# Performance work log

Hardware: AMD Instinct MI355X
Metric: run time of the kernel (lower is better)

The kernel has to match this reference:

```python
import jax, jax.numpy as jnp
import numpy as np

B, T, D, H, NHASH, BS, L, DFF = 4, 4096, 512, 8, 4, 64, 4, 2048
DH = D // H           # 64
NB = T // BS          # 64 buckets per hash round
MASK_VAL = -5e4       # TOKEN_SELF_ATTN_VALUE from reformer-pytorch


def setup_inputs() -> dict:
    key = jax.random.key(0)
    ks = jax.random.split(key, 8)
    s = D ** -0.5
    return {
        "src": jax.random.normal(ks[0], (B, T, D), jnp.float32),
        "rotations": jax.random.normal(ks[1], (L, DH, NHASH, NB // 2), jnp.float32),
        "Wqk": jax.random.normal(ks[2], (L, D, D), jnp.float32) * s,
        "Wv": jax.random.normal(ks[3], (L, D, D), jnp.float32) * s,
        "Wout": jax.random.normal(ks[4], (L, D, D), jnp.float32) * s,
        "bout": jnp.zeros((L, D), jnp.float32),
        "W1": jax.random.normal(ks[5], (L, DFF, D), jnp.float32) * s,
        "b1": jnp.zeros((L, DFF), jnp.float32),
        "W2": jax.random.normal(ks[6], (L, D, DFF), jnp.float32) * (DFF ** -0.5),
        "b2": jnp.zeros((L, D), jnp.float32),
        "g2": jnp.ones((L, D), jnp.float32),
        "be2": jnp.zeros((L, D), jnp.float32),
        "gf": jnp.ones((D,), jnp.float32),
        "bf": jnp.zeros((D,), jnp.float32),
    }


def _ln(x, g, b, eps=1e-6):
    m = x.mean(-1, keepdims=True)
    v = ((x - m) ** 2).mean(-1, keepdims=True)
    return (x - m) * jax.lax.rsqrt(v + eps) * g + b


def _look_one_back(x):
    # concat each chunk with the previous chunk along the within-chunk axis
    return jnp.concatenate([x, jnp.roll(x, 1, axis=1)], axis=2)


def _lsh_attention(qk, v, rot):
    # qk, v: (bh, T, DH); rot: (DH, NHASH, NB//2). Shared-QK LSH attention.
    bh = qk.shape[0]
    rotated = jnp.einsum('btf,fhr->bhtr', qk, rot)               # (bh,NHASH,T,NB/2)
    full = jnp.concatenate([rotated, -rotated], axis=-1)          # (bh,NHASH,T,NB)
    buckets = jnp.argmax(full, axis=-1)                           # (bh,NHASH,T)
    buckets = buckets + (jnp.arange(NHASH) * NB)[None, :, None]   # offset per round
    buckets = buckets.reshape(bh, NHASH * T)

    ticker = jnp.arange(NHASH * T)
    bt = buckets * T + (ticker % T)                               # unique sort keys
    sticker = jnp.argsort(bt, axis=-1)                            # sort positions
    undo = jnp.argsort(sticker, axis=-1)
    st = sticker % T                                              # original positions

    sqk = jnp.take_along_axis(qk, st[..., None], axis=1)          # (bh,NHASH*T,DH)
    sv = jnp.take_along_axis(v, st[..., None], axis=1)

    C = NHASH * NB                                                # chunks
    bq_t = st.reshape(bh, C, BS)
    bqk = sqk.reshape(bh, C, BS, DH)
    bv = sv.reshape(bh, C, BS, DH)

    bq = bqk
    bk = bqk / jnp.maximum(jnp.linalg.norm(bqk, axis=-1, keepdims=True), 1e-12)
    bk = _look_one_back(bk)                                       # (bh,C,2*BS,DH)
    bv = _look_one_back(bv)
    bkv_t = _look_one_back(bq_t)                                  # (bh,C,2*BS)

    dots = jnp.einsum('bcie,bcje->bcij', bq, bk) * (DH ** -0.5)   # (bh,C,BS,2BS)
    self_mask = bq_t[:, :, :, None] == bkv_t[:, :, None, :]
    dots = jnp.where(self_mask, MASK_VAL, dots)

    lse = jax.scipy.special.logsumexp(dots, axis=-1, keepdims=True)
    probs = jnp.exp(dots - lse)
    bo = jnp.einsum('bcij,bcje->bcie', probs, bv)                 # (bh,C,BS,DH)

    so = bo.reshape(bh, NHASH * T, DH)
    slog = lse.reshape(bh, NHASH * T)
    o = jnp.take_along_axis(so, undo[..., None], axis=1).reshape(bh, NHASH, T, DH)
    lg = jnp.take_along_axis(slog, undo, axis=1).reshape(bh, NHASH, T, 1)
    w = jnp.exp(lg - jax.scipy.special.logsumexp(lg, axis=1, keepdims=True))
    return jnp.sum(o * w, axis=1)                                 # (bh,T,DH)


def _split_heads(x):
    return x.reshape(B, T, H, DH).transpose(0, 2, 1, 3).reshape(B * H, T, DH)


def _merge_heads(x):
    return x.reshape(B, H, T, DH).transpose(0, 2, 1, 3).reshape(B, T, D)


def reference(src, rotations, Wqk, Wv, Wout, bout, W1, b1, W2, b2, g2, be2, gf, bf):
    x = src
    for i in range(L):
        # LSH self-attention (post-norm path: norm1 is never applied in source)
        qk = _split_heads(x @ Wqk[i].T)
        v = _split_heads(x @ Wv[i].T)
        att = _merge_heads(_lsh_attention(qk, v, rotations[i]))
        att = att @ Wout[i].T + bout[i]
        x = x + att
        # positionalwise FFN + residual + norm2
        ff = jax.nn.relu(x @ W1[i].T + b1[i]) @ W2[i].T + b2[i]
        x = _ln(x + ff, g2[i], be2[i])
    return _ln(x, gf, bf)
```

## Files before the change

### kernel.cpp

```cpp
#include <hip/hip_runtime.h>
#include <math.h>

#define TT    4096
#define DD    512
#define HH    8
#define DHH   64
#define NH    4
#define LLAY  4
#define DFFN  2048
#define BHH   32
#define NC    256
#define MROWS 16384

typedef __attribute__((ext_vector_type(8))) short s16x8;
typedef __attribute__((ext_vector_type(4))) float f32x4;
typedef unsigned short ushort_t;

union U4 { unsigned u[4]; s16x8 v; };

__device__ __forceinline__ unsigned short f2bf(float f) {
    unsigned u = __float_as_uint(f);
    unsigned r = (u + 0x7FFFu + ((u >> 16) & 1u)) >> 16;
    return (unsigned short)r;
}
__device__ __forceinline__ float bf2f(unsigned short h) {
    return __uint_as_float(((unsigned)h) << 16);
}

__device__ __forceinline__ void xcd_swz(int& bx, int& by) {
    const int gx = gridDim.x;
    const int nwg = gx * gridDim.y;
    const int flat = by * gx + bx;
    const int q = nwg >> 3;
    const int swz = (flat & 7) * q + (flat >> 3);
    bx = swz % gx;
    by = swz / gx;
}

__global__ __launch_bounds__(256) void gemm_bf3_k(
    const ushort_t* __restrict__ Ah, const ushort_t* __restrict__ Al, int lda,
    const ushort_t* __restrict__ Wh, const ushort_t* __restrict__ Wl, int ldw,
    const float* __restrict__ bias, const float* __restrict__ resid,
    float* __restrict__ outf, ushort_t* __restrict__ outh, ushort_t* __restrict__ outl,
    unsigned* __restrict__ outp,
    int M, int N, int K, int relu)
{
    __shared__ __align__(16) ushort_t lds[2][4 * 128 * 32];
    const int tid  = threadIdx.x;
    const int lane = tid & 63;
    const int wv   = tid >> 6;
    const int wm   = wv >> 1, wn = wv & 1;
    int bx = blockIdx.x, by = blockIdx.y;
    xcd_swz(bx, by);
    const int row0 = by * 128, col0 = bx * 128;
    const int g    = lane >> 4;
    const int srow0 = wv * 32;

    f32x4 acc[4][4];
#pragma unroll
    for (int mi = 0; mi < 4; mi++)
#pragma unroll
        for (int ni = 0; ni < 4; ni++) acc[mi][ni] = (f32x4)(0.f);

    auto STAGE = [&](int buf, int k0) {
#pragma unroll
        for (int ii = 0; ii < 2; ii++) {
            const int r   = srow0 + ii * 16 + (lane >> 2);
            const int ug  = (((lane & 3) ^ ((r >> 1) & 3)) << 3);
            const size_t ga = (size_t)(row0 + r) * lda + k0 + ug;
            const size_t gw = (size_t)(col0 + r) * ldw + k0 + ug;
            const int lo  = (srow0 + ii * 16) * 32;
            __builtin_amdgcn_global_load_lds(
                (const __attribute__((address_space(1))) void*)(Ah + ga),
                (__attribute__((address_space(3))) void*)&lds[buf][0 * 4096 + lo], 16, 0, 0);
            __builtin_amdgcn_global_load_lds(
                (const __attribute__((address_space(1))) void*)(Al + ga),
                (__attribute__((address_space(3))) void*)&lds[buf][1 * 4096 + lo], 16, 0, 0);
            __builtin_amdgcn_global_load_lds(
                (const __attribute__((address_space(1))) void*)(Wh + gw),
                (__attribute__((address_space(3))) void*)&lds[buf][2 * 4096 + lo], 16, 0, 0);
            __builtin_amdgcn_global_load_lds(
                (const __attribute__((address_space(1))) void*)(Wl + gw),
                (__attribute__((address_space(3))) void*)&lds[buf][3 * 4096 + lo], 16, 0, 0);
        }
    };

    const int nt = K >> 5;
    STAGE(0, 0);

    for (int t = 0; t < nt; ++t) {
        const int cur = t & 1;
        if (t + 1 < nt) {
            STAGE(cur ^ 1, (t + 1) << 5);
            asm volatile("s_waitcnt vmcnt(8)" ::: "memory");
        } else {
            asm volatile("s_waitcnt vmcnt(0)" ::: "memory");
        }
        __builtin_amdgcn_s_barrier();
        __builtin_amdgcn_sched_barrier(0);

        s16x8 ah[4], al[4], wh[4], wl[4];
#pragma unroll
        for (int mi = 0; mi < 4; mi++) {
            const int m  = wm * 64 + mi * 16 + (lane & 15);
            const int pu = ((g ^ ((m >> 1) & 3)) << 3);
            ah[mi] = *(const s16x8*)&lds[cur][0 * 4096 + m * 32 + pu];
            al[mi] = *(const s16x8*)&lds[cur][1 * 4096 + m * 32 + pu];
            const int n  = wn * 64 + mi * 16 + (lane & 15);
            const int pn = ((g ^ ((n >> 1) & 3)) << 3);
            wh[mi] = *(const s16x8*)&lds[cur][2 * 4096 + n * 32 + pn];
            wl[mi] = *(const s16x8*)&lds[cur][3 * 4096 + n * 32 + pn];
        }
#pragma unroll
        for (int mi = 0; mi < 4; mi++)
#pragma unroll
            for (int ni = 0; ni < 4; ni++) {
                acc[mi][ni] = __builtin_amdgcn_mfma_f32_16x16x32_bf16(ah[mi], wh[ni], acc[mi][ni], 0, 0, 0);
                acc[mi][ni] = __builtin_amdgcn_mfma_f32_16x16x32_bf16(al[mi], wh[ni], acc[mi][ni], 0, 0, 0);
                acc[mi][ni] = __builtin_amdgcn_mfma_f32_16x16x32_bf16(ah[mi], wl[ni], acc[mi][ni], 0, 0, 0);
            }

        __builtin_amdgcn_sched_barrier(0);
        __builtin_amdgcn_s_barrier();
    }

#pragma unroll
    for (int mi = 0; mi < 4; mi++) {
#pragma unroll
        for (int ni = 0; ni < 4; ni++) {
#pragma unroll
            for (int r = 0; r < 4; r++) {
                const int row = row0 + wm * 64 + mi * 16 + g * 4 + r;
                const int col = col0 + wn * 64 + ni * 16 + (lane & 15);
                float v = acc[mi][ni][r];
                if (bias)  v += bias[col];
                if (relu)  v = fmaxf(v, 0.f);
                if (resid) v += resid[(size_t)row * N + col];
                if (outf)  outf[(size_t)row * N + col] = v;
                if (outh) {
                    unsigned short h = f2bf(v);
                    outh[(size_t)row * N + col] = h;
                    outl[(size_t)row * N + col] = f2bf(v - bf2f(h));
                }
                if (outp) {
                    unsigned short h = f2bf(v);
                    outp[(size_t)row * N + col] =
                        (unsigned)h | ((unsigned)f2bf(v - bf2f(h)) << 16);
                }
            }
        }
    }
}

__global__ __launch_bounds__(256) void gemm_bf6_k(
    const ushort_t* __restrict__ A1, const ushort_t* __restrict__ A2,
    const ushort_t* __restrict__ A3, int lda,
    const ushort_t* __restrict__ W1, const ushort_t* __restrict__ W2,
    const ushort_t* __restrict__ W3,
    float* __restrict__ outf, unsigned* __restrict__ outp, int M, int N, int K)
{
    __shared__ __align__(16) ushort_t lds[6 * 128 * 32];
    const int tid  = threadIdx.x;
    const int lane = tid & 63;
    const int wv   = tid >> 6;
    const int wm   = wv >> 1, wn = wv & 1;
    int bx = blockIdx.x, by = blockIdx.y;
    xcd_swz(bx, by);
    const int row0 = by * 128, col0 = bx * 128;
    const int g    = lane >> 4;

    f32x4 acc[4][4];
#pragma unroll
    for (int mi = 0; mi < 4; mi++)
#pragma unroll
        for (int ni = 0; ni < 4; ni++) acc[mi][ni] = (f32x4)(0.f);

    const int srow0 = wv * 32;

    for (int k0 = 0; k0 < K; k0 += 32) {
        __syncthreads();
#pragma unroll
        for (int ii = 0; ii < 2; ii++) {
            const int r   = srow0 + ii * 16 + (lane >> 2);
            const int ug  = (((lane & 3) ^ ((r >> 1) & 3)) << 3);
            const size_t ga = (size_t)(row0 + r) * lda + k0 + ug;
            const size_t gw = (size_t)(col0 + r) * K   + k0 + ug;
            const int lo  = (srow0 + ii * 16) * 32;
            __builtin_amdgcn_global_load_lds(
                (const __attribute__((address_space(1))) void*)(A1 + ga),
                (__attribute__((address_space(3))) void*)&lds[0 * 4096 + lo], 16, 0, 0);
            __builtin_amdgcn_global_load_lds(
                (const __attribute__((address_space(1))) void*)(A2 + ga),
                (__attribute__((address_space(3))) void*)&lds[1 * 4096 + lo], 16, 0, 0);
            __builtin_amdgcn_global_load_lds(
                (const __attribute__((address_space(1))) void*)(A3 + ga),
                (__attribute__((address_space(3))) void*)&lds[2 * 4096 + lo], 16, 0, 0);
            __builtin_amdgcn_global_load_lds(
                (const __attribute__((address_space(1))) void*)(W1 + gw),
                (__attribute__((address_space(3))) void*)&lds[3 * 4096 + lo], 16, 0, 0);
            __builtin_amdgcn_global_load_lds(
                (const __attribute__((address_space(1))) void*)(W2 + gw),
                (__attribute__((address_space(3))) void*)&lds[4 * 4096 + lo], 16, 0, 0);
            __builtin_amdgcn_global_load_lds(
                (const __attribute__((address_space(1))) void*)(W3 + gw),
                (__attribute__((address_space(3))) void*)&lds[5 * 4096 + lo], 16, 0, 0);
        }
        __syncthreads();

        s16x8 a1[4], a2[4], a3[4], w1[4], w2[4], w3[4];
#pragma unroll
        for (int mi = 0; mi < 4; mi++) {
            const int m  = wm * 64 + mi * 16 + (lane & 15);
            const int pu = ((g ^ ((m >> 1) & 3)) << 3);
            a1[mi] = *(const s16x8*)&lds[0 * 4096 + m * 32 + pu];
            a2[mi] = *(const s16x8*)&lds[1 * 4096 + m * 32 + pu];
            a3[mi] = *(const s16x8*)&lds[2 * 4096 + m * 32 + pu];
            const int n  = wn * 64 + mi * 16 + (lane & 15);
            const int pn = ((g ^ ((n >> 1) & 3)) << 3);
            w1[mi] = *(const s16x8*)&lds[3 * 4096 + n * 32 + pn];
            w2[mi] = *(const s16x8*)&lds[4 * 4096 + n * 32 + pn];
            w3[mi] = *(const s16x8*)&lds[5 * 4096 + n * 32 + pn];
        }
#pragma unroll
        for (int mi = 0; mi < 4; mi++)
#pragma unroll
            for (int ni = 0; ni < 4; ni++) {
                acc[mi][ni] = __builtin_amdgcn_mfma_f32_16x16x32_bf16(a1[mi], w1[ni], acc[mi][ni], 0, 0, 0);
                acc[mi][ni] = __builtin_amdgcn_mfma_f32_16x16x32_bf16(a2[mi], w1[ni], acc[mi][ni], 0, 0, 0);
                acc[mi][ni] = __builtin_amdgcn_mfma_f32_16x16x32_bf16(a1[mi], w2[ni], acc[mi][ni], 0, 0, 0);
                acc[mi][ni] = __builtin_amdgcn_mfma_f32_16x16x32_bf16(a2[mi], w2[ni], acc[mi][ni], 0, 0, 0);
                acc[mi][ni] = __builtin_amdgcn_mfma_f32_16x16x32_bf16(a1[mi], w3[ni], acc[mi][ni], 0, 0, 0);
                acc[mi][ni] = __builtin_amdgcn_mfma_f32_16x16x32_bf16(a3[mi], w1[ni], acc[mi][ni], 0, 0, 0);
            }
    }

#pragma unroll
    for (int mi = 0; mi < 4; mi++) {
#pragma unroll
        for (int ni = 0; ni < 4; ni++) {
#pragma unroll
            for (int r = 0; r < 4; r++) {
                const int row = row0 + wm * 64 + mi * 16 + g * 4 + r;
                const int col = col0 + wn * 64 + ni * 16 + (lane & 15);
                float v = acc[mi][ni][r];
                outf[(size_t)row * N + col] = v;
                unsigned short h = f2bf(v);
                outp[(size_t)row * N + col] =
                    (unsigned)h | ((unsigned)f2bf(v - bf2f(h)) << 16);
            }
        }
    }
}

__global__ __launch_bounds__(256) void cvt_k(
    const float* __restrict__ in, ushort_t* __restrict__ o1,
    ushort_t* __restrict__ o2, ushort_t* __restrict__ o3, int n4)
{
    int i = blockIdx.x * 256 + threadIdx.x;
    if (i >= n4) return;
    float4 v = ((const float4*)in)[i];
    float vv[4] = {v.x, v.y, v.z, v.w};
    union { unsigned short us[4]; ushort4 v4; } H, L, M;
#pragma unroll
    for (int q = 0; q < 4; q++) {
        unsigned short a = f2bf(vv[q]);
        float r1 = vv[q] - bf2f(a);
        unsigned short b = f2bf(r1);
        H.us[q] = a; L.us[q] = b;
        M.us[q] = f2bf(r1 - bf2f(b));
    }
    ((ushort4*)o1)[i] = H.v4;
    ((ushort4*)o2)[i] = L.v4;
    if (o3) ((ushort4*)o3)[i] = M.v4;
}

__global__ __launch_bounds__(256) void bucket_k(
    const float* __restrict__ qk, const float* __restrict__ rot,
    int* __restrict__ bkt)
{
    __shared__ float rs[NH][64][32];
    const int bh = blockIdx.y;
    const int t = blockIdx.x * 256 + threadIdx.x;
    for (int i = threadIdx.x; i < NH * 64 * 32; i += 256) {
        int r = i >> 11, f = (i >> 5) & 63, j = i & 31;
        rs[r][f][j] = rot[(f * NH + r) * 32 + j];
    }
    __syncthreads();
    const int b = bh >> 3, h = bh & 7;
    const float* q = qk + ((size_t)(b * TT + t)) * DD + h * DHH;
    float qv[64];
#pragma unroll
    for (int f4 = 0; f4 < 16; f4++) {
        float4 tmp = ((const float4*)q)[f4];
        qv[f4 * 4 + 0] = tmp.x; qv[f4 * 4 + 1] = tmp.y;
        qv[f4 * 4 + 2] = tmp.z; qv[f4 * 4 + 3] = tmp.w;
    }
    for (int r = 0; r < NH; r++) {
        float rv[32];
#pragma unroll
        for (int j = 0; j < 32; j++) rv[j] = 0.f;
        for (int f = 0; f < 64; f++) {
            float qf = qv[f];
#pragma unroll
            for (int j = 0; j < 32; j++) rv[j] = fmaf(qf, rs[r][f][j], rv[j]);
        }
        float best = rv[0];
        int bi = 0;
#pragma unroll
        for (int j = 1; j < 32; j++) { if (rv[j] > best) { best = rv[j]; bi = j; } }
#pragma unroll
        for (int j = 0; j < 32; j++) { float v = -rv[j]; if (v > best) { best = v; bi = 32 + j; } }
        bkt[((size_t)bh * NH + r) * TT + t] = bi;
    }
}

__global__ __launch_bounds__(256) void sort_k(
    const int* __restrict__ bkt, int* __restrict__ st)
{
    __shared__ int lb[TT];
    __shared__ unsigned short cnt[128][64];
    __shared__ int base[64];
    const int r = blockIdx.x, bh = blockIdx.y;
    const int tid = threadIdx.x;
    const int* src = bkt + ((size_t)bh * NH + r) * TT;

    const int4* s4 = (const int4*)src;
    int4* l4 = (int4*)lb;
#pragma unroll
    for (int q = 0; q < 4; q++) l4[tid + q * 256] = s4[tid + q * 256];
    unsigned* cz = (unsigned*)cnt;
#pragma unroll
    for (int q = 0; q < 16; q++) cz[tid + q * 256] = 0;
    __syncthreads();

    if (tid < 128) {
        for (int it = 0; it < 32; it++) {
            int bb = lb[tid * 32 + it];
            cnt[tid][bb]++;
        }
    }
    __syncthreads();

    if (tid < 64) {
        const int bb = tid;
        int run = 0;
        for (int s = 0; s < 128; s++) {
            int t = cnt[s][bb];
            cnt[s][bb] = (unsigned short)run;
            run += t;
        }
        int inc = run;
#pragma unroll
        for (int off = 1; off < 64; off <<= 1) {
            int n = __shfl_up(inc, off, 64);
            if (tid >= off) inc += n;
        }
        base[bb] = inc - run;
    }
    __syncthreads();

    if (tid < 128) {
        int* dst = st + (size_t)bh * (NH * TT) + (size_t)r * TT;
        for (int it = 0; it < 32; it++) {
            int t = tid * 32 + it;
            int bb = lb[t];
            int pos = base[bb] + (int)cnt[tid][bb];
            cnt[tid][bb]++;
            dst[pos] = t;
        }
    }
}

__global__ __launch_bounds__(256, 2) void attn_k(
    const unsigned* __restrict__ qkp, const unsigned* __restrict__ vp,
    const int* __restrict__ st, float* __restrict__ obuf,
    float* __restrict__ lseb, int bh0)
{
    __shared__ __align__(16) ushort_t ksh[128 * 72];
    __shared__ __align__(16) ushort_t ksl[128 * 72];
    __shared__ __align__(16) unsigned vsp[128 * 66];
    __shared__ float invn[128];
    __shared__ int   tks[128];

    const int c   = blockIdx.x;
    const int bhl = blockIdx.y;
    const int bh  = bh0 + bhl;
    const int b   = bh >> 3, h = bh & 7;
    const int tid = threadIdx.x;
    const int* stb = st + (size_t)bh * (NH * TT);

    if (tid < 128) {
        int cc = (tid < 64) ? c : ((c + NC - 1) & (NC - 1));
        tks[tid] = stb[cc * 64 + (tid & 63)];
    }
    __syncthreads();

    {
        const int row = tid >> 1, c0 = (tid & 1) * 32;
        const int t = tks[row];
        const uint4* kg = (const uint4*)(qkp + ((size_t)(b * TT + t)) * DD + h * DHH + c0);
        const uint4* vg = (const uint4*)(vp  + ((size_t)(b * TT + t)) * DD + h * DHH + c0);
        unsigned kp[32];
        uint4 vq[8];
        float ss = 0.f;
#pragma unroll
        for (int q = 0; q < 8; q++) {
            uint4 kq = kg[q];
            kp[4 * q + 0] = kq.x; kp[4 * q + 1] = kq.y;
            kp[4 * q + 2] = kq.z; kp[4 * q + 3] = kq.w;
            vq[q] = vg[q];
        }
#pragma unroll
        for (int e = 0; e < 32; e++) {
            float f = __uint_as_float(kp[e] << 16) + __uint_as_float(kp[e] & 0xffff0000u);
            ss = fmaf(f, f, ss);
        }
        ss += __shfl_xor(ss, 1);
        if ((tid & 1) == 0) invn[row] = 1.0f / fmaxf(sqrtf(ss), 1e-12f);

        unsigned hw[16], lw[16];
#pragma unroll
        for (int e = 0; e < 16; e++) {
            hw[e] = (kp[2 * e] & 0xffffu) | (kp[2 * e + 1] << 16);
            lw[e] = (kp[2 * e] >> 16) | (kp[2 * e + 1] & 0xffff0000u);
        }
        uint4* kdh = (uint4*)&ksh[row * 72 + c0];
        uint4* kdl = (uint4*)&ksl[row * 72 + c0];
#pragma unroll
        for (int q = 0; q < 4; q++) {
            kdh[q] = make_uint4(hw[4 * q], hw[4 * q + 1], hw[4 * q + 2], hw[4 * q + 3]);
            kdl[q] = make_uint4(lw[4 * q], lw[4 * q + 1], lw[4 * q + 2], lw[4 * q + 3]);
        }
        uint2* vd = (uint2*)&vsp[row * 66 + c0];
#pragma unroll
        for (int q = 0; q < 8; q++) {
            vd[2 * q]     = make_uint2(vq[q].x, vq[q].y);
            vd[2 * q + 1] = make_uint2(vq[q].z, vq[q].w);
        }
    }
    __syncthreads();

    const int lane = tid & 63;
    const int wv   = tid >> 6;
    const int cc16 = lane & 15;
    const int g    = lane >> 4;
    const int rr   = c >> 6;

    f32x4 stt[8];
#pragma unroll
    for (int jt = 0; jt < 8; jt++) stt[jt] = (f32x4)(0.f);

    const int qrow = wv * 16 + cc16;
#pragma unroll
    for (int ks = 0; ks < 2; ks++) {
        s16x8 qh = *(const s16x8*)&ksh[qrow * 72 + ks * 32 + g * 8];
        s16x8 ql = *(const s16x8*)&ksl[qrow * 72 + ks * 32 + g * 8];
#pragma unroll
        for (int jt = 0; jt < 8; jt++) {
            const int krow = jt * 16 + cc16;
            s16x8 ah = *(const s16x8*)&ksh[krow * 72 + ks * 32 + g * 8];
            s16x8 al = *(const s16x8*)&ksl[krow * 72 + ks * 32 + g * 8];
            stt[jt] = __builtin_amdgcn_mfma_f32_16x16x32_bf16(ah, qh, stt[jt], 0, 0, 0);
            stt[jt] = __builtin_amdgcn_mfma_f32_16x16x32_bf16(al, qh, stt[jt], 0, 0, 0);
            stt[jt] = __builtin_amdgcn_mfma_f32_16x16x32_bf16(ah, ql, stt[jt], 0, 0, 0);
        }
    }

    const int tqi = tks[wv * 16 + cc16];
    float m = -INFINITY;
#pragma unroll
    for (int jt = 0; jt < 8; jt++) {
#pragma unroll
        for (int r4 = 0; r4 < 4; r4++) {
            const int j = jt * 16 + g * 4 + r4;
            float d = stt[jt][r4] * invn[j] * 0.125f;
            if (tqi == tks[j]) d = -5e4f;
            stt[jt][r4] = d;
            m = fmaxf(m, d);
        }
    }
    m = fmaxf(m, __shfl_xor(m, 16));
    m = fmaxf(m, __shfl_xor(m, 32));
    float s = 0.f;
#pragma unroll
    for (int jt = 0; jt < 8; jt++) {
#pragma unroll
        for (int r4 = 0; r4 < 4; r4++) {
            float e = expf(stt[jt][r4] - m);
            stt[jt][r4] = e;
            s += e;
        }
    }
    s += __shfl_xor(s, 16);
    s += __shfl_xor(s, 32);
    const float is = 1.0f / s;
    if (g == 0) lseb[((size_t)bh * NH + rr) * TT + tqi] = m + logf(s);

    unsigned ph[8][2], pl[8][2];
#pragma unroll
    for (int jt = 0; jt < 8; jt++) {
#pragma unroll
        for (int w2 = 0; w2 < 2; w2++) {
            float p0 = stt[jt][2 * w2] * is;
            float p1 = stt[jt][2 * w2 + 1] * is;
            unsigned short h0 = f2bf(p0), h1 = f2bf(p1);
            ph[jt][w2] = (unsigned)h0 | ((unsigned)h1 << 16);
            pl[jt][w2] = (unsigned)f2bf(p0 - bf2f(h0)) | ((unsigned)f2bf(p1 - bf2f(h1)) << 16);
        }
    }

    f32x4 occ[4];
#pragma unroll
    for (int nt = 0; nt < 4; nt++) occ[nt] = (f32x4)(0.f);

    const int srcLow  = ((g & 1) << 5) + cc16;
    const int srcHigh = srcLow + 16;
    const bool hiT = (lane & 32) != 0;

#pragma unroll
    for (int ks = 0; ks < 4; ks++) {
        U4 Phi, Plo;
        {
            unsigned a0 = (unsigned)__shfl((int)ph[2 * ks][0], srcLow);
            unsigned a1 = (unsigned)__shfl((int)ph[2 * ks][1], srcLow);
            unsigned a2 = (unsigned)__shfl((int)ph[2 * ks][0], srcHigh);
            unsigned a3 = (unsigned)__shfl((int)ph[2 * ks][1], srcHigh);
            unsigned b0 = (unsigned)__shfl((int)ph[2 * ks + 1][0], srcLow);
            unsigned b1 = (unsigned)__shfl((int)ph[2 * ks + 1][1], srcLow);
            unsigned b2 = (unsigned)__shfl((int)ph[2 * ks + 1][0], srcHigh);
            unsigned b3 = (unsigned)__shfl((int)ph[2 * ks + 1][1], srcHigh);
            Phi.u[0] = hiT ? b0 : a0; Phi.u[1] = hiT ? b1 : a1;
            Phi.u[2] = hiT ? b2 : a2; Phi.u[3] = hiT ? b3 : a3;
            unsigned c0 = (unsigned)__shfl((int)pl[2 * ks][0], srcLow);
            unsigned c1 = (unsigned)__shfl((int)pl[2 * ks][1], srcLow);
            unsigned c2 = (unsigned)__shfl((int)pl[2 * ks][0], srcHigh);
            unsigned c3 = (unsigned)__shfl((int)pl[2 * ks][1], srcHigh);
            unsigned d0 = (unsigned)__shfl((int)pl[2 * ks + 1][0], srcLow);
            unsigned d1 = (unsigned)__shfl((int)pl[2 * ks + 1][1], srcLow);
            unsigned d2 = (unsigned)__shfl((int)pl[2 * ks + 1][0], srcHigh);
            unsigned d3 = (unsigned)__shfl((int)pl[2 * ks + 1][1], srcHigh);
            Plo.u[0] = hiT ? d0 : c0; Plo.u[1] = hiT ? d1 : c1;
            Plo.u[2] = hiT ? d2 : c2; Plo.u[3] = hiT ? d3 : c3;
        }
#pragma unroll
        for (int nt = 0; nt < 4; nt++) {
            unsigned u[8];
#pragma unroll
            for (int e = 0; e < 8; e++)
                u[e] = vsp[(32 * ks + 8 * g + e) * 66 + nt * 16 + cc16];
            U4 Vh, Vl;
#pragma unroll
            for (int m2 = 0; m2 < 4; m2++) {
                Vh.u[m2] = (u[2 * m2] & 0xffffu) | (u[2 * m2 + 1] << 16);
                Vl.u[m2] = (u[2 * m2] >> 16) | (u[2 * m2 + 1] & 0xffff0000u);
            }
            occ[nt] = __builtin_amdgcn_mfma_f32_16x16x32_bf16(Phi.v, Vh.v, occ[nt], 0, 0, 0);
            occ[nt] = __builtin_amdgcn_mfma_f32_16x16x32_bf16(Plo.v, Vh.v, occ[nt], 0, 0, 0);
            occ[nt] = __builtin_amdgcn_mfma_f32_16x16x32_bf16(Phi.v, Vl.v, occ[nt], 0, 0, 0);
        }
    }

#pragma unroll
    for (int r4 = 0; r4 < 4; r4++) {
        const int i = wv * 16 + g * 4 + r4;
        const int ti = tks[i];
        float* dst = obuf + (((size_t)bhl * NH + rr) * TT + ti) * DHH + cc16;
        dst[0]  = occ[0][r4];
        dst[16] = occ[1][r4];
        dst[32] = occ[2][r4];
        dst[48] = occ[3][r4];
    }
}

__global__ __launch_bounds__(256) void combine_k(
    const float* __restrict__ obuf, const float* __restrict__ lseb,
    ushort_t* __restrict__ att, int bh0)
{
    int idx = blockIdx.x * 256 + threadIdx.x;
    int d = idx & 63;
    int t = (idx >> 6) & (TT - 1);
    int bhl = idx >> 18;
    int bh = bh0 + bhl;
    float l0 = lseb[((size_t)bh * NH + 0) * TT + t];
    float l1 = lseb[((size_t)bh * NH + 1) * TT + t];
    float l2 = lseb[((size_t)bh * NH + 2) * TT + t];
    float l3 = lseb[((size_t)bh * NH + 3) * TT + t];
    float m = fmaxf(fmaxf(l0, l1), fmaxf(l2, l3));
    float e0 = expf(l0 - m), e1 = expf(l1 - m), e2 = expf(l2 - m), e3 = expf(l3 - m);
    float inv = 1.0f / (e0 + e1 + e2 + e3);
    float o0 = obuf[(((size_t)bhl * NH + 0) * TT + t) * DHH + d];
    float o1 = obuf[(((size_t)bhl * NH + 1) * TT + t) * DHH + d];
    float o2 = obuf[(((size_t)bhl * NH + 2) * TT + t) * DHH + d];
    float o3 = obuf[(((size_t)bhl * NH + 3) * TT + t) * DHH + d];
    float o = (e0 * o0 + e1 * o1 + e2 * o2 + e3 * o3) * inv;
    int b = bh >> 3, h = bh & 7;
    size_t base = (size_t)(b * TT + t) * 1024 + h * DHH + d;
    unsigned short hi = f2bf(o);
    att[base]       = hi;
    att[base + 512] = f2bf(o - bf2f(hi));
}

__global__ __launch_bounds__(64) void ln_k(
    const float* __restrict__ in, const float* __restrict__ g,
    const float* __restrict__ be, float* __restrict__ out,
    ushort_t* __restrict__ oh, ushort_t* __restrict__ ol,
    ushort_t* __restrict__ ol2)
{
    const int row = blockIdx.x;
    const int tid = threadIdx.x;
    const float* x = in + (size_t)row * DD;
    float4 a = *(const float4*)(x + tid * 8);
    float4 b = *(const float4*)(x + tid * 8 + 4);
    float s = a.x + a.y + a.z + a.w + b.x + b.y + b.z + b.w;
#pragma unroll
    for (int o = 32; o >= 1; o >>= 1) s += __shfl_xor(s, o, 64);
    float mean = s * (1.0f / 512.0f);
    float dx[8];
    dx[0] = a.x - mean; dx[1] = a.y - mean; dx[2] = a.z - mean; dx[3] = a.w - mean;
    dx[4] = b.x - mean; dx[5] = b.y - mean; dx[6] = b.z - mean; dx[7] = b.w - mean;
    float ss = 0.f;
#pragma unroll
    for (int q = 0; q < 8; q++) ss += dx[q] * dx[q];
#pragma unroll
    for (int o = 32; o >= 1; o >>= 1) ss += __shfl_xor(ss, o, 64);
    float var = ss * (1.0f / 512.0f);
    float inv = 1.0f / sqrtf(var + 1e-6f);
    const float* gp = g + tid * 8;
    const float* bp = be + tid * 8;
    float y[8];
#pragma unroll
    for (int q = 0; q < 8; q++) y[q] = dx[q] * inv * gp[q] + bp[q];
    float* yp = out + (size_t)row * DD + tid * 8;
    *(float4*)(yp)     = make_float4(y[0], y[1], y[2], y[3]);
    *(float4*)(yp + 4) = make_float4(y[4], y[5], y[6], y[7]);
    if (oh) {
        union { unsigned short us[8]; ushort4 v4[2]; } H, L, M;
#pragma unroll
        for (int q = 0; q < 8; q++) {
            unsigned short h = f2bf(y[q]);
            float r1 = y[q] - bf2f(h);
            unsigned short l = f2bf(r1);
            H.us[q] = h; L.us[q] = l;
            M.us[q] = f2bf(r1 - bf2f(l));
        }
        size_t e = (size_t)row * DD + tid * 8;
        *(ushort4*)(oh + e)      = H.v4[0];
        *(ushort4*)(oh + e + 4)  = H.v4[1];
        *(ushort4*)(ol + e)      = L.v4[0];
        *(ushort4*)(ol + e + 4)  = L.v4[1];
        *(ushort4*)(ol2 + e)     = M.v4[0];
        *(ushort4*)(ol2 + e + 4) = M.v4[1];
    }
}

extern "C" void kernel_launch(void* const* d_in, const int* in_sizes, int n_in,
                              void* d_out, int out_size, void* d_ws, size_t ws_size,
                              hipStream_t stream)
{
    const float* src  = (const float*)d_in[0];
    const float* rots = (const float*)d_in[1];
    const float* Wqk  = (const float*)d_in[2];
    const float* Wv   = (const float*)d_in[3];
    const float* Wout = (const float*)d_in[4];
    const float* bout = (const float*)d_in[5];
    const float* W1   = (const float*)d_in[6];
    const float* b1   = (const float*)d_in[7];
    const float* W2   = (const float*)d_in[8];
    const float* b2   = (const float*)d_in[9];
    const float* g2   = (const float*)d_in[10];
    const float* be2  = (const float*)d_in[11];
    const float* gf   = (const float*)d_in[12];
    const float* bf   = (const float*)d_in[13];
    float* out = (float*)d_out;

    char* w = (char*)d_ws;
    const size_t SZ_X = (size_t)MROWS * DD * 4;
    const size_t XHALF = (size_t)MROWS * DD;
    float*    x     = (float*)(w);
    ushort_t* xs    = (ushort_t*)(w + SZ_X);
    ushort_t* xh    = xs;
    ushort_t* xl    = xs + XHALF;
    ushort_t* xl2   = xs + 2 * XHALF;
    char*     p     = w + SZ_X + 3 * XHALF * 2;
    float*    qkb   = (float*)(p);
    ushort_t* attb  = (ushort_t*)(p);
    unsigned* vp    = (unsigned*)(p + SZ_X);
    unsigned* qkp   = (unsigned*)(p + 2 * SZ_X);
    float*    obuf  = (float*)(p + 3 * SZ_X);
    ushort_t* h1h   = (ushort_t*)(p);
    ushort_t* h1l   = (ushort_t*)(p + 2 * SZ_X);
    ushort_t* wb    = (ushort_t*)(p + 4 * SZ_X);
    char*     tail  = p + 4 * SZ_X + 6029312 * 2;
    int*      bkt   = (int*)(tail);
    int*      st    = (int*)(tail + (size_t)BHH * NH * TT * 4);
    float*    lseb  = (float*)(tail + 2 * (size_t)BHH * NH * TT * 4);

    ushort_t* wvh = wb;            ushort_t* wvl = wb + 262144;
    ushort_t* woh = wb + 524288;   ushort_t* wol = wb + 786432;
    ushort_t* w1h = wb + 1048576;  ushort_t* w1l = wb + 2097152;
    ushort_t* w2h = wb + 3145728;  ushort_t* w2l = wb + 4194304;
    ushort_t* wq1 = wb + 5242880;  ushort_t* wq2 = wb + 5505024;
    ushort_t* wq3 = wb + 5767168;

    hipMemcpyAsync(x, src, SZ_X, hipMemcpyDeviceToDevice, stream);
    cvt_k<<<(MROWS * DD / 4 + 255) / 256, 256, 0, stream>>>(src, xh, xl, xl2, MROWS * DD / 4);

    for (int i = 0; i < LLAY; i++) {
        const float* Wqk_i = Wqk + (size_t)i * DD * DD;
        const float* Wv_i  = Wv  + (size_t)i * DD * DD;
        const float* Wout_i= Wout+ (size_t)i * DD * DD;
        const float* bout_i= bout+ (size_t)i * DD;
        const float* W1_i  = W1  + (size_t)i * DFFN * DD;
        const float* b1_i  = b1  + (size_t)i * DFFN;
        const float* W2_i  = W2  + (size_t)i * DD * DFFN;
        const float* b2_i  = b2  + (size_t)i * DD;
        const float* g2_i  = g2  + (size_t)i * DD;
        const float* be2_i = be2 + (size_t)i * DD;
        const float* rot_i = rots + (size_t)i * DHH * NH * 32;

        cvt_k<<<(262144 / 4 + 255) / 256, 256, 0, stream>>>(Wqk_i, wq1, wq2, wq3, 262144 / 4);
        cvt_k<<<(262144 / 4 + 255) / 256, 256, 0, stream>>>(Wv_i, wvh, wvl, nullptr, 262144 / 4);
        cvt_k<<<(262144 / 4 + 255) / 256, 256, 0, stream>>>(Wout_i, woh, wol, nullptr, 262144 / 4);
        cvt_k<<<(1048576 / 4 + 255) / 256, 256, 0, stream>>>(W1_i, w1h, w1l, nullptr, 1048576 / 4);
        cvt_k<<<(1048576 / 4 + 255) / 256, 256, 0, stream>>>(W2_i, w2h, w2l, nullptr, 1048576 / 4);

        gemm_bf6_k<<<dim3(4, 128), 256, 0, stream>>>(xh, xl, xl2, DD, wq1, wq2, wq3,
                                                     qkb, qkp, MROWS, DD, DD);
        gemm_bf3_k<<<dim3(4, 128), 256, 0, stream>>>(xh, xl, DD, wvh, wvl, DD,
                                                     nullptr, nullptr,
                                                     nullptr, nullptr, nullptr, vp,
                                                     MROWS, DD, DD, 0);
        bucket_k<<<dim3(16, BHH), 256, 0, stream>>>(qkb, rot_i, bkt);
        sort_k<<<dim3(NH, BHH), 256, 0, stream>>>(bkt, st);

        for (int s = 0; s < 4; s++) {
            attn_k<<<dim3(NC, 8), 256, 0, stream>>>(qkp, vp, st, obuf, lseb, s * 8);
            combine_k<<<8192, 256, 0, stream>>>(obuf, lseb, attb, s * 8);
        }

        gemm_bf3_k<<<dim3(4, 128), 256, 0, stream>>>(attb, attb + 512, 1024, woh, wol, DD,
                                                     bout_i, x, x, xh, xl, nullptr,
                                                     MROWS, DD, DD, 0);
        gemm_bf3_k<<<dim3(16, 128), 256, 0, stream>>>(xh, xl, DD, w1h, w1l, DD,
                                                      b1_i, nullptr,
                                                      nullptr, h1h, h1l, nullptr,
                                                      MROWS, DFFN, DD, 1);
        gemm_bf3_k<<<dim3(4, 128), 256, 0, stream>>>(h1h, h1l, DFFN, w2h, w2l, DFFN,
                                                     b2_i, x,
                                                     x, nullptr, nullptr, nullptr,
                                                     MROWS, DD, DFFN, 0);
        ln_k<<<MROWS, 64, 0, stream>>>(x, g2_i, be2_i, x, xh, xl, xl2);
    }
    ln_k<<<MROWS, 64, 0, stream>>>(x, gf, bf, out, nullptr, nullptr, nullptr);
}
```

Baseline: 3.081 ms.

## Batch weight conversions into one kernel, fuse input copy, raise MFMA wave priority

The five per-layer weight conversion launches become a single cvtw_k launch that picks its source and destination by block range. The initial device-to-device copy of src is folded into the input conversion kernel through a new output pointer. s_setprio(1) is wrapped around the MFMA blocks in the GEMM and attention kernels so the hardware favours matrix-issuing waves. Together these cut launch overhead and one full pass over the input. The priority hints may change how waves interleave and could help or hurt.

```diff
diff --git a/kernel.cpp b/kernel.cpp
--- a/kernel.cpp
+++ b/kernel.cpp
@@ -111,6 +111,7 @@
             wh[mi] = *(const s16x8*)&lds[cur][2 * 4096 + n * 32 + pn];
             wl[mi] = *(const s16x8*)&lds[cur][3 * 4096 + n * 32 + pn];
         }
+        __builtin_amdgcn_s_setprio(1);
 #pragma unroll
         for (int mi = 0; mi < 4; mi++)
 #pragma unroll
@@ -119,6 +120,7 @@
                 acc[mi][ni] = __builtin_amdgcn_mfma_f32_16x16x32_bf16(al[mi], wh[ni], acc[mi][ni], 0, 0, 0);
                 acc[mi][ni] = __builtin_amdgcn_mfma_f32_16x16x32_bf16(ah[mi], wl[ni], acc[mi][ni], 0, 0, 0);
             }
+        __builtin_amdgcn_s_setprio(0);
 
         __builtin_amdgcn_sched_barrier(0);
         __builtin_amdgcn_s_barrier();
@@ -221,6 +223,7 @@
             w2[mi] = *(const s16x8*)&lds[4 * 4096 + n * 32 + pn];
             w3[mi] = *(const s16x8*)&lds[5 * 4096 + n * 32 + pn];
         }
+        __builtin_amdgcn_s_setprio(1);
 #pragma unroll
         for (int mi = 0; mi < 4; mi++)
 #pragma unroll
@@ -232,6 +235,7 @@
                 acc[mi][ni] = __builtin_amdgcn_mfma_f32_16x16x32_bf16(a1[mi], w3[ni], acc[mi][ni], 0, 0, 0);
                 acc[mi][ni] = __builtin_amdgcn_mfma_f32_16x16x32_bf16(a3[mi], w1[ni], acc[mi][ni], 0, 0, 0);
             }
+        __builtin_amdgcn_s_setprio(0);
     }
 
 #pragma unroll
@@ -254,10 +258,48 @@
 
 __global__ __launch_bounds__(256) void cvt_k(
     const float* __restrict__ in, ushort_t* __restrict__ o1,
-    ushort_t* __restrict__ o2, ushort_t* __restrict__ o3, int n4)
+    ushort_t* __restrict__ o2, ushort_t* __restrict__ o3,
+    float* __restrict__ ocopy, int n4)
 {
     int i = blockIdx.x * 256 + threadIdx.x;
     if (i >= n4) return;
+    float4 v = ((const float4*)in)[i];
+    if (ocopy) ((float4*)ocopy)[i] = v;
+    float vv[4] = {v.x, v.y, v.z, v.w};
+    union { unsigned short us[4]; ushort4 v4; } H, L, M;
+#pragma unroll
+    for (int q = 0; q < 4; q++) {
+        unsigned short a = f2bf(vv[q]);
+        float r1 = vv[q] - bf2f(a);
+        unsigned short b = f2bf(r1);
+        H.us[q] = a; L.us[q] = b;
+        M.us[q] = f2bf(r1 - bf2f(b));
+    }
+    ((ushort4*)o1)[i] = H.v4;
+    ((ushort4*)o2)[i] = L.v4;
+    if (o3) ((ushort4*)o3)[i] = M.v4;
+}
+
+__global__ __launch_bounds__(256) void cvtw_k(
+    const float* __restrict__ Wqk_i, const float* __restrict__ Wv_i,
+    const float* __restrict__ Wout_i, const float* __restrict__ W1_i,
+    const float* __restrict__ W2_i,
+    ushort_t* __restrict__ wq1, ushort_t* __restrict__ wq2, ushort_t* __restrict__ wq3,
+    ushort_t* __restrict__ wvh, ushort_t* __restrict__ wvl,
+    ushort_t* __restrict__ woh, ushort_t* __restrict__ wol,
+    ushort_t* __restrict__ w1h, ushort_t* __restrict__ w1l,
+    ushort_t* __restrict__ w2h, ushort_t* __restrict__ w2l)
+{
+    const int blk = blockIdx.x;
+    const float* in;
+    ushort_t *o1, *o2, *o3 = nullptr;
+    int i;
+    if (blk < 256)       { in = Wqk_i;  o1 = wq1; o2 = wq2; o3 = wq3; i = blk * 256; }
+    else if (blk < 512)  { in = Wv_i;   o1 = wvh; o2 = wvl; i = (blk - 256) * 256; }
+    else if (blk < 768)  { in = Wout_i; o1 = woh; o2 = wol; i = (blk - 512) * 256; }
+    else if (blk < 1792) { in = W1_i;   o1 = w1h; o2 = w1l; i = (blk - 768) * 256; }
+    else                 { in = W2_i;   o1 = w2h; o2 = w2l; i = (blk - 1792) * 256; }
+    i += threadIdx.x;
     float4 v = ((const float4*)in)[i];
     float vv[4] = {v.x, v.y, v.z, v.w};
     union { unsigned short us[4]; ushort4 v4; } H, L, M;
@@ -455,6 +497,7 @@
     for (int ks = 0; ks < 2; ks++) {
         s16x8 qh = *(const s16x8*)&ksh[qrow * 72 + ks * 32 + g * 8];
         s16x8 ql = *(const s16x8*)&ksl[qrow * 72 + ks * 32 + g * 8];
+        __builtin_amdgcn_s_setprio(1);
 #pragma unroll
         for (int jt = 0; jt < 8; jt++) {
             const int krow = jt * 16 + cc16;
@@ -464,6 +507,7 @@
             stt[jt] = __builtin_amdgcn_mfma_f32_16x16x32_bf16(al, qh, stt[jt], 0, 0, 0);
             stt[jt] = __builtin_amdgcn_mfma_f32_16x16x32_bf16(ah, ql, stt[jt], 0, 0, 0);
         }
+        __builtin_amdgcn_s_setprio(0);
     }
 
     const int tqi = tks[wv * 16 + cc16];
@@ -554,9 +598,11 @@
                 Vh.u[m2] = (u[2 * m2] & 0xffffu) | (u[2 * m2 + 1] << 16);
                 Vl.u[m2] = (u[2 * m2] >> 16) | (u[2 * m2 + 1] & 0xffff0000u);
             }
+            __builtin_amdgcn_s_setprio(1);
             occ[nt] = __builtin_amdgcn_mfma_f32_16x16x32_bf16(Phi.v, Vh.v, occ[nt], 0, 0, 0);
             occ[nt] = __builtin_amdgcn_mfma_f32_16x16x32_bf16(Plo.v, Vh.v, occ[nt], 0, 0, 0);
             occ[nt] = __builtin_amdgcn_mfma_f32_16x16x32_bf16(Phi.v, Vl.v, occ[nt], 0, 0, 0);
+            __builtin_amdgcn_s_setprio(0);
         }
     }
 
@@ -702,8 +748,8 @@
     ushort_t* wq1 = wb + 5242880;  ushort_t* wq2 = wb + 5505024;
     ushort_t* wq3 = wb + 5767168;
 
-    hipMemcpyAsync(x, src, SZ_X, hipMemcpyDeviceToDevice, stream);
-    cvt_k<<<(MROWS * DD / 4 + 255) / 256, 256, 0, stream>>>(src, xh, xl, xl2, MROWS * DD / 4);
+    cvt_k<<<(MROWS * DD / 4 + 255) / 256, 256, 0, stream>>>(src, xh, xl, xl2, x,
+                                                            MROWS * DD / 4);
 
     for (int i = 0; i < LLAY; i++) {
         const float* Wqk_i = Wqk + (size_t)i * DD * DD;
@@ -718,11 +764,9 @@
         const float* be2_i = be2 + (size_t)i * DD;
         const float* rot_i = rots + (size_t)i * DHH * NH * 32;
 
-        cvt_k<<<(262144 / 4 + 255) / 256, 256, 0, stream>>>(Wqk_i, wq1, wq2, wq3, 262144 / 4);
-        cvt_k<<<(262144 / 4 + 255) / 256, 256, 0, stream>>>(Wv_i, wvh, wvl, nullptr, 262144 / 4);
-        cvt_k<<<(262144 / 4 + 255) / 256, 256, 0, stream>>>(Wout_i, woh, wol, nullptr, 262144 / 4);
-        cvt_k<<<(1048576 / 4 + 255) / 256, 256, 0, stream>>>(W1_i, w1h, w1l, nullptr, 1048576 / 4);
-        cvt_k<<<(1048576 / 4 + 255) / 256, 256, 0, stream>>>(W2_i, w2h, w2l, nullptr, 1048576 / 4);
+        cvtw_k<<<2816, 256, 0, stream>>>(Wqk_i, Wv_i, Wout_i, W1_i, W2_i,
+                                         wq1, wq2, wq3, wvh, wvl, woh, wol,
+                                         w1h, w1l, w2h, w2l);
 
         gemm_bf6_k<<<dim3(4, 128), 256, 0, stream>>>(xh, xl, xl2, DD, wq1, wq2, wq3,
                                                      qkb, qkp, MROWS, DD, DD);
```

New measurement: 3.038 ms. About the same (-1.4%).
